# Optimization experiments

Measured on AMD Instinct MI355X. Metric: run time of the kernel, lower is better.

Reference implementation:

```python
import jax, jax.numpy as jnp
import numpy as np

HEADS = 6
K = 3       # kernel_size
PAD = 1     # padding (stride = 1, so AvgPool is identity and h=H, w=W)


def setup_inputs() -> dict:
    key = jax.random.key(0)
    ks = jax.random.split(key, 6)
    B, H, W, C = 8, 56, 56, 192
    k4h = (K ** 4) * HEADS  # 486
    s = 0.02
    return {
        "x":  jax.random.normal(ks[0], (B, H, W, C), jnp.float32),
        # weights stored as (in, out), i.e. transpose of torch nn.Linear.weight
        "Wv": jax.random.normal(ks[1], (C, C), jnp.float32) * s,
        "Wa": jax.random.normal(ks[2], (C, k4h), jnp.float32) * s,
        "ba": jnp.zeros((k4h,), jnp.float32),
        "Wp": jax.random.normal(ks[3], (C, C), jnp.float32) * s,
        "bp": jnp.zeros((C,), jnp.float32),
    }


def _outlook(x, Wv, Wa, ba, Wp, bp):
    B, H, W, C = x.shape
    hd = C // HEADS
    scale = hd ** (-0.5)
    k2 = K * K
    hw = H * W

    # v projection (no bias), to NCHW
    v = jnp.einsum("bhwc,cd->bdhw", x, Wv)                       # [B,C,H,W]

    # unfold: extract k x k local windows (same ordering as nn.Unfold: C, ki, kj)
    vp = jnp.pad(v, ((0, 0), (0, 0), (PAD, PAD), (PAD, PAD)))
    patches = jnp.stack(
        [vp[:, :, i:i + H, j:j + W] for i in range(K) for j in range(K)],
        axis=2,
    )                                                            # [B,C,k2,H,W]
    v = patches.reshape(B, HEADS, hd, k2, hw).transpose(0, 1, 4, 3, 2)  # [B,h,hw,k2,hd]

    # attention weights: dense predicted per location (pool is identity, stride=1)
    a = x.reshape(B, hw, C) @ Wa + ba                            # [B,hw,heads*k2*k2]
    a = a.reshape(B, hw, HEADS, k2, k2).transpose(0, 2, 1, 3, 4)  # [B,h,hw,k2,k2]
    a = jax.nn.softmax(a * scale, axis=-1)

    out = jnp.einsum("bnpkq,bnpqd->bnpkd", a, v)                 # [B,h,hw,k2,hd]

    # fold (col2im): scatter-add overlapping windows back, stride=1
    cols = out.transpose(0, 1, 4, 3, 2).reshape(B, C, K, K, H, W)
    acc = jnp.zeros((B, C, H + 2 * PAD, W + 2 * PAD), x.dtype)
    for i in range(K):
        for j in range(K):
            acc = acc.at[:, :, i:i + H, j:j + W].add(cols[:, :, i, j])
    y = acc[:, :, PAD:PAD + H, PAD:PAD + W].transpose(0, 2, 3, 1)  # [B,H,W,C]

    return y @ Wp + bp


def reference(x, Wv, Wa, ba, Wp, bp):
    return _outlook(x, Wv, Wa, ba, Wp, bp)
```

## Files before the change

kernel.cpp:

```cpp
#include <hip/hip_runtime.h>
#include <hip/hip_bf16.h>
#include <cstdint>

#define DI __device__ __forceinline__

typedef __attribute__((ext_vector_type(8))) short short8;
typedef __attribute__((ext_vector_type(4))) float f32x4;

DI float bflo(uint32_t u) { return __builtin_bit_cast(float, (uint32_t)(u << 16)); }
DI float bfhi(uint32_t u) { return __builtin_bit_cast(float, (uint32_t)(u & 0xffff0000u)); }
DI float bf2f(uint16_t u) { return __builtin_bit_cast(float, (uint32_t)((uint32_t)u << 16)); }
DI uint32_t cvtpk(float lo, float hi) {
    uint32_t r;
    asm("v_cvt_pk_bf16_f32 %0, %1, %2" : "=v"(r) : "v"(lo), "v"(hi));
    return r;
}
DI void gload16(const void* g, void* s) {
    __builtin_amdgcn_global_load_lds(
        (const __attribute__((address_space(1))) uint32_t*)g,
        (__attribute__((address_space(3))) uint32_t*)s, 16, 0, 0);
}
DI int xcd_swizzle(int orig, int nwg) {
    const int q = nwg >> 3, r = nwg & 7;
    const int x = orig & 7, i = orig >> 3;
    return (x < r ? x * (q + 1) : r * (q + 1) + (x - r) * q) + i;
}

constexpr int BATCH = 8, HH_IMG = 56, WW_IMG = 56, C = 192;
constexpr int HEADS = 6, HD = 32, NA = 486;
constexpr int MROWS = BATCH * HH_IMG * WW_IMG;
constexpr int KK = 192;
constexpr int TILE_B  = 49152;
constexpr int PANEL_B = 49152;


__global__ __launch_bounds__(256) void prep_all(const float* __restrict__ x,
                                                const float* __restrict__ Wv,
                                                const float* __restrict__ Wa,
                                                const float* __restrict__ Wp,
                                                uint8_t* __restrict__ xbf,
                                                uint8_t* __restrict__ WT) {
    const int bid = blockIdx.x;
    if (bid < 2352) {
        const int g = bid * 256 + threadIdx.x;
        const int m = g / 24, cc = g % 24;
        const int ks = cc >> 2, lg = cc & 3;
        const float* src = x + (size_t)m * KK + cc * 8;
        const float4 v0 = *(const float4*)src;
        const float4 v1 = *(const float4*)(src + 4);
        uint4 o;
        o.x = cvtpk(v0.x, v0.y); o.y = cvtpk(v0.z, v0.w);
        o.z = cvtpk(v1.x, v1.y); o.w = cvtpk(v1.z, v1.w);
        const size_t off = (size_t)(m >> 7) * PANEL_B +
                           ((((m >> 4) & 7) * 6 + ks) * 64 + (lg << 4) + (m & 15)) * 16;
        *(uint4*)(xbf + off) = o;
    } else {
        const int tid = (bid - 2352) * 256 + threadIdx.x;
        const int s = tid % 24, rem = tid / 24;
        const int p = rem & 127, tile = rem >> 7;
        const int lc = (p >> 5) * 32 + 2 * (p & 15) + ((p >> 4) & 1);
        const int u  = (tile < 6 ? tile : tile - 6) * 128 + lc;
        const float* src = nullptr; int nc = 0, col = 0;
        if (tile < 6) {
            if (u < 192)      { src = Wv; nc = 192; col = u; }
            else if (u < 678) { src = Wa; nc = NA;  col = u - 192; }
        } else {
            if (u < 192)      { src = Wp; nc = 192; col = u; }
        }
        const int k0 = s * 8;
        uint32_t d[4];
#pragma unroll
        for (int e = 0; e < 4; ++e) {
            const float f0 = src ? src[(size_t)(k0 + 2 * e) * nc + col]     : 0.f;
            const float f1 = src ? src[(size_t)(k0 + 2 * e + 1) * nc + col] : 0.f;
            d[e] = cvtpk(f0, f1);
        }
        const int sb = (s * 16) ^ ((p & 7) << 4);
        *(uint4*)(WT + (size_t)tile * TILE_B + p * 384 + sb) =
            make_uint4(d[0], d[1], d[2], d[3]);
    }
}

template <bool OUT_DUAL, int NT>
__global__ __launch_bounds__(256, 2) void gemm_fr(
    const uint8_t* __restrict__ Afr,
    const uint8_t* __restrict__ WT,
    uint16_t* __restrict__ vOut, uint16_t* __restrict__ alogOut,
    const float* __restrict__ bias,
    float* __restrict__ outf) {
    __shared__ __align__(16) uint8_t sm[TILE_B];
    const int t    = threadIdx.x;
    const int wgid = xcd_swizzle(blockIdx.x, gridDim.x);
    const int mg   = wgid / NT, ti = wgid - mg * NT;
    const int m0   = mg * 128;
    const int l    = t & 63, wid = t >> 6;
    const int wr   = wid >> 1, wc = wid & 1;
    const int lr   = l & 15, lg = l >> 4;

    const uint8_t* wt = WT + (size_t)ti * TILE_B;
#pragma unroll
    for (int i = 0; i < 12; ++i) {
        const int off = wid * 12288 + i * 1024;
        gload16(wt + off + l * 16, sm + off);
    }

    const uint8_t* ap = Afr + (size_t)mg * PANEL_B;
    short8 aR[6][4];
#pragma unroll
    for (int ks = 0; ks < 6; ++ks)
#pragma unroll
        for (int mr = 0; mr < 4; ++mr) {
            const int r = wr * 4 + mr;
            aR[ks][mr] = *(const short8*)(ap + (size_t)(((r * 6 + ks) * 64) + l) * 16);
        }
    __syncthreads();

    f32x4 acc[4][4];
#pragma unroll
    for (int mr = 0; mr < 4; ++mr)
#pragma unroll
        for (int nr = 0; nr < 4; ++nr) acc[mr][nr] = f32x4{0.f, 0.f, 0.f, 0.f};
#pragma unroll
    for (int ks = 0; ks < 6; ++ks) {
        const int cb = ks * 64 + lg * 16;
        short8 b[4];
#pragma unroll
        for (int nr = 0; nr < 4; ++nr) {
            const int rn = wc * 64 + nr * 16 + lr;
            b[nr] = *(const short8*)(sm + rn * 384 + (cb ^ ((rn & 7) << 4)));
        }
#pragma unroll
        for (int mr = 0; mr < 4; ++mr)
#pragma unroll
            for (int nr = 0; nr < 4; ++nr)
                acc[mr][nr] = __builtin_amdgcn_mfma_f32_16x16x32_bf16(
                    aR[ks][mr], b[nr], acc[mr][nr], 0, 0, 0);
    }

    const int gcol0 = ti * 128 + wc * 64;
#pragma unroll
    for (int pr = 0; pr < 2; ++pr) {
        if (OUT_DUAL) {
            const bool isv = gcol0 < 192;
            uint16_t* dst = isv ? vOut : alogOut;
            const int nc  = isv ? 192 : NA;
            const int c   = (isv ? gcol0 : gcol0 - 192) + pr * 32 + 2 * lr;
            if (c < nc) {
                const float be = isv ? 0.f : bias[c];
                const float bo = isv ? 0.f : bias[c + 1];
#pragma unroll
                for (int mr = 0; mr < 4; ++mr) {
                    const size_t rb = (size_t)(m0 + wr * 64 + mr * 16 + lg * 4);
#pragma unroll
                    for (int j = 0; j < 4; ++j)
                        *(uint32_t*)(dst + (rb + j) * nc + c) =
                            cvtpk(acc[mr][2 * pr][j] + be, acc[mr][2 * pr + 1][j] + bo);
                }
            }
        } else {
            const int c = gcol0 + pr * 32 + 2 * lr;
            if (c < 192) {
                const float be = bias[c], bo = bias[c + 1];
#pragma unroll
                for (int mr = 0; mr < 4; ++mr) {
                    const size_t rb = (size_t)(m0 + wr * 64 + mr * 16 + lg * 4);
#pragma unroll
                    for (int j = 0; j < 4; ++j)
                        *(float2*)(outf + (rb + j) * 192 + c) =
                            make_float2(acc[mr][2 * pr][j] + be,
                                        acc[mr][2 * pr + 1][j] + bo);
                }
            }
        }
    }
}

constexpr int TH = 4, TW = 8;
constexpr int HALO_W = TW + 4;
constexpr int VSTR = C + 8;

__global__ __launch_bounds__(192) void attn_fold25(const uint16_t* __restrict__ v,
                                                   const uint16_t* __restrict__ alog,
                                                   uint8_t* __restrict__ ypre) {
    __shared__ uint16_t vl[96][VSTR];
    const int b   = blockIdx.z;
    const int ty0 = blockIdx.y * TH, tx0 = blockIdx.x * TW;
    const int t   = threadIdx.x;

#pragma unroll
    for (int it = 0; it < 12; ++it) {
        const int f  = t + it * 192;
        const int px = f / 24, c8 = (f % 24) * 8;
        const int hy = px / HALO_W, hx = px % HALO_W;
        const int y = ty0 + hy - 2, x = tx0 + hx - 2;
        uint4 val = make_uint4(0u, 0u, 0u, 0u);
        if ((unsigned)y < HH_IMG && (unsigned)x < WW_IMG)
            val = *(const uint4*)&v[(((size_t)b * HH_IMG + y) * WW_IMG + x) * C + c8];
        *(uint4*)&vl[px][c8] = val;
    }

    const int n   = t % HEADS, pxl = t / HEADS;
    const int py  = pxl / TW, px_ = pxl % TW;
    const int Py  = ty0 + py, Px = tx0 + px_;
    const float scl2 = 0.17677669529663687f * 1.4426950408889634f;

    float cw[5][5] = {};
#pragma unroll
    for (int i = 0; i < 3; ++i)
#pragma unroll
        for (int j = 0; j < 3; ++j) {
            const int sy = Py - i + 1, sx = Px - j + 1;
            if ((unsigned)sy < HH_IMG && (unsigned)sx < WW_IMG) {
                const uint16_t* ap = alog + (((size_t)b * HH_IMG + sy) * WW_IMG + sx) * NA
                                   + n * 81 + (i * 3 + j) * 9;
                float w[9], s = 0.f;
#pragma unroll
                for (int q = 0; q < 9; ++q) {
                    w[q] = __builtin_amdgcn_exp2f(bf2f(ap[q]) * scl2);
                    s += w[q];
                }
                const float inv = __builtin_amdgcn_rcpf(s);
#pragma unroll
                for (int qi = 0; qi < 3; ++qi)
#pragma unroll
                    for (int qj = 0; qj < 3; ++qj)
                        cw[qi - i + 2][qj - j + 2] += w[qi * 3 + qj] * inv;
            }
        }
    __syncthreads();

    float acc[HD] = {};
#pragma unroll
    for (int dy = 0; dy < 5; ++dy)
#pragma unroll
        for (int dx = 0; dx < 5; ++dx) {
            const float wq = cw[dy][dx];
            const uint16_t* vp = &vl[(py + dy) * HALO_W + (px_ + dx)][n * HD];
#pragma unroll
            for (int v8 = 0; v8 < 4; ++v8) {
                const uint4 raw = *(const uint4*)&vp[v8 * 8];
                const uint32_t r0 = raw.x, r1 = raw.y, r2 = raw.z, r3 = raw.w;
                acc[v8*8+0] = fmaf(wq, bflo(r0), acc[v8*8+0]);
                acc[v8*8+1] = fmaf(wq, bfhi(r0), acc[v8*8+1]);
                acc[v8*8+2] = fmaf(wq, bflo(r1), acc[v8*8+2]);
                acc[v8*8+3] = fmaf(wq, bfhi(r1), acc[v8*8+3]);
                acc[v8*8+4] = fmaf(wq, bflo(r2), acc[v8*8+4]);
                acc[v8*8+5] = fmaf(wq, bfhi(r2), acc[v8*8+5]);
                acc[v8*8+6] = fmaf(wq, bflo(r3), acc[v8*8+6]);
                acc[v8*8+7] = fmaf(wq, bfhi(r3), acc[v8*8+7]);
            }
        }

    const int Pidx = (b * HH_IMG + Py) * WW_IMG + Px;
    uint8_t* pb = ypre + (size_t)(Pidx >> 7) * PANEL_B +
                  ((((Pidx >> 4) & 7) * 6 + n) * 64 + (Pidx & 15)) * 16;
#pragma unroll
    for (int g2 = 0; g2 < 4; ++g2) {
        uint4 o;
        o.x = cvtpk(acc[g2 * 8 + 0], acc[g2 * 8 + 1]);
        o.y = cvtpk(acc[g2 * 8 + 2], acc[g2 * 8 + 3]);
        o.z = cvtpk(acc[g2 * 8 + 4], acc[g2 * 8 + 5]);
        o.w = cvtpk(acc[g2 * 8 + 6], acc[g2 * 8 + 7]);
        *(uint4*)(pb + g2 * 256) = o;
    }
}

extern "C" void kernel_launch(void* const* d_in, const int* in_sizes, int n_in,
                              void* d_out, int out_size, void* d_ws, size_t ws_size,
                              hipStream_t stream) {
    const float* x  = (const float*)d_in[0];
    const float* Wv = (const float*)d_in[1];
    const float* Wa = (const float*)d_in[2];
    const float* ba = (const float*)d_in[3];
    const float* Wp = (const float*)d_in[4];
    const float* bp = (const float*)d_in[5];
    float* out = (float*)d_out;

    uint16_t* v    = (uint16_t*)d_ws;
    uint16_t* alog = v + (size_t)MROWS * C;
    uint8_t*  ypre = (uint8_t*)(alog + (size_t)MROWS * NA);
    uint8_t*  WT   = ypre + (size_t)(MROWS / 128) * PANEL_B;
    uint8_t*  xbf  = WT + 8 * (size_t)TILE_B;

    prep_all<<<2448, 256, 0, stream>>>(x, Wv, Wa, Wp, xbf, WT);
    gemm_fr<true, 6><<<(MROWS / 128) * 6, 256, 0, stream>>>(
        xbf, WT, v, alog, ba, nullptr);
    attn_fold25<<<dim3(WW_IMG / TW, HH_IMG / TH, BATCH), dim3(192), 0, stream>>>(
        v, alog, ypre);
    gemm_fr<false, 2><<<(MROWS / 128) * 2, 256, 0, stream>>>(
        ypre, WT + 6 * (size_t)TILE_B, nullptr, nullptr, bp, out);
}
```

Baseline: 61.64 us.

## Fuse output projection GEMM into attention-fold kernel and pad attention logits

The final Wp projection is now done inside the attention/fold kernel. Each block stages its 32 bf16 output rows in LDS and runs MFMA against a pre-fragmented Wp read from global memory, which removes the ypre round trip and one kernel launch. The attention logits are padded from 81 to 88 per head (528 columns) so each window's 9 logits load as two 16-byte vector loads instead of scalar bf16 loads. In exchange, the fused kernel needs more LDS and registers, which may lower occupancy, and every block re-reads Wp fragments from global memory.

```diff
diff --git a/kernel.cpp b/kernel.cpp
--- a/kernel.cpp
+++ b/kernel.cpp
@@ -9,7 +9,6 @@
 
 DI float bflo(uint32_t u) { return __builtin_bit_cast(float, (uint32_t)(u << 16)); }
 DI float bfhi(uint32_t u) { return __builtin_bit_cast(float, (uint32_t)(u & 0xffff0000u)); }
-DI float bf2f(uint16_t u) { return __builtin_bit_cast(float, (uint32_t)((uint32_t)u << 16)); }
 DI uint32_t cvtpk(float lo, float hi) {
     uint32_t r;
     asm("v_cvt_pk_bf16_f32 %0, %1, %2" : "=v"(r) : "v"(lo), "v"(hi));
@@ -28,18 +27,22 @@
 
 constexpr int BATCH = 8, HH_IMG = 56, WW_IMG = 56, C = 192;
 constexpr int HEADS = 6, HD = 32, NA = 486;
+constexpr int NAP = 528;
 constexpr int MROWS = BATCH * HH_IMG * WW_IMG;
 constexpr int KK = 192;
 constexpr int TILE_B  = 49152;
 constexpr int PANEL_B = 49152;
-
+constexpr int WTB_B   = 73728;
 
 __global__ __launch_bounds__(256) void prep_all(const float* __restrict__ x,
                                                 const float* __restrict__ Wv,
                                                 const float* __restrict__ Wa,
                                                 const float* __restrict__ Wp,
+                                                const float* __restrict__ ba,
                                                 uint8_t* __restrict__ xbf,
-                                                uint8_t* __restrict__ WT) {
+                                                uint8_t* __restrict__ WT,
+                                                uint8_t* __restrict__ WTB,
+                                                float* __restrict__ baP) {
     const int bid = blockIdx.x;
     if (bid < 2352) {
         const int g = bid * 256 + threadIdx.x;
@@ -54,18 +57,20 @@
         const size_t off = (size_t)(m >> 7) * PANEL_B +
                            ((((m >> 4) & 7) * 6 + ks) * 64 + (lg << 4) + (m & 15)) * 16;
         *(uint4*)(xbf + off) = o;
-    } else {
-        const int tid = (bid - 2352) * 256 + threadIdx.x;
+        return;
+    }
+    const int tid = (bid - 2352) * 256 + threadIdx.x;
+    if (tid < 18432) {
         const int s = tid % 24, rem = tid / 24;
         const int p = rem & 127, tile = rem >> 7;
         const int lc = (p >> 5) * 32 + 2 * (p & 15) + ((p >> 4) & 1);
-        const int u  = (tile < 6 ? tile : tile - 6) * 128 + lc;
+        const int u  = tile * 128 + lc;
         const float* src = nullptr; int nc = 0, col = 0;
-        if (tile < 6) {
-            if (u < 192)      { src = Wv; nc = 192; col = u; }
-            else if (u < 678) { src = Wa; nc = NA;  col = u - 192; }
-        } else {
-            if (u < 192)      { src = Wp; nc = 192; col = u; }
+        if (u < 192) { src = Wv; nc = 192; col = u; }
+        else if (u < 720) {
+            const int up = u - 192;
+            const int head = up / 88, r88 = up - head * 88;
+            if (r88 < 81) { src = Wa; nc = NA; col = head * 81 + r88; }
         }
         const int k0 = s * 8;
         uint32_t d[4];
@@ -78,20 +83,37 @@
         const int sb = (s * 16) ^ ((p & 7) << 4);
         *(uint4*)(WT + (size_t)tile * TILE_B + p * 384 + sb) =
             make_uint4(d[0], d[1], d[2], d[3]);
-    }
-}
-
-template <bool OUT_DUAL, int NT>
+    } else if (tid < 18432 + 4608) {
+        const int g = tid - 18432;
+        const int l = g & 63, gg = g >> 6;
+        const int ks = gg % 6, nrIdx = gg / 6;
+        const int pp = nrIdx >> 1, h = nrIdx & 1;
+        const int col = pp * 32 + 2 * (l & 15) + h;
+        const int k0  = ks * 32 + (l >> 4) * 8;
+        uint32_t d[4];
+#pragma unroll
+        for (int e = 0; e < 4; ++e) {
+            const float f0 = Wp[(size_t)(k0 + 2 * e) * 192 + col];
+            const float f1 = Wp[(size_t)(k0 + 2 * e + 1) * 192 + col];
+            d[e] = cvtpk(f0, f1);
+        }
+        *(uint4*)(WTB + (size_t)g * 16) = make_uint4(d[0], d[1], d[2], d[3]);
+    } else if (tid < 18432 + 4608 + NAP) {
+        const int pc = tid - 18432 - 4608;
+        const int head = pc / 88, r88 = pc - head * 88;
+        baP[pc] = (r88 < 81) ? ba[head * 81 + r88] : 0.f;
+    }
+}
+
 __global__ __launch_bounds__(256, 2) void gemm_fr(
     const uint8_t* __restrict__ Afr,
     const uint8_t* __restrict__ WT,
-    uint16_t* __restrict__ vOut, uint16_t* __restrict__ alogOut,
-    const float* __restrict__ bias,
-    float* __restrict__ outf) {
+    uint16_t* __restrict__ zOut, uint16_t* __restrict__ alogP,
+    const float* __restrict__ baP) {
     __shared__ __align__(16) uint8_t sm[TILE_B];
     const int t    = threadIdx.x;
     const int wgid = xcd_swizzle(blockIdx.x, gridDim.x);
-    const int mg   = wgid / NT, ti = wgid - mg * NT;
+    const int mg   = wgid / 6, ti = wgid - mg * 6;
     const int m0   = mg * 128;
     const int l    = t & 63, wid = t >> 6;
     const int wr   = wid >> 1, wc = wid & 1;
@@ -140,35 +162,27 @@
     const int gcol0 = ti * 128 + wc * 64;
 #pragma unroll
     for (int pr = 0; pr < 2; ++pr) {
-        if (OUT_DUAL) {
-            const bool isv = gcol0 < 192;
-            uint16_t* dst = isv ? vOut : alogOut;
-            const int nc  = isv ? 192 : NA;
-            const int c   = (isv ? gcol0 : gcol0 - 192) + pr * 32 + 2 * lr;
-            if (c < nc) {
-                const float be = isv ? 0.f : bias[c];
-                const float bo = isv ? 0.f : bias[c + 1];
+        const int uc = gcol0 + pr * 32 + 2 * lr;
+        if (uc < 192) {
+#pragma unroll
+            for (int mr = 0; mr < 4; ++mr) {
+                const size_t rb = (size_t)(m0 + wr * 64 + mr * 16 + lg * 4);
+#pragma unroll
+                for (int j = 0; j < 4; ++j)
+                    *(uint32_t*)(zOut + (rb + j) * 192 + uc) =
+                        cvtpk(acc[mr][2 * pr][j], acc[mr][2 * pr + 1][j]);
+            }
+        } else {
+            const int pc = uc - 192;
+            if (pc < NAP) {
+                const float be = baP[pc], bo = baP[pc + 1];
 #pragma unroll
                 for (int mr = 0; mr < 4; ++mr) {
                     const size_t rb = (size_t)(m0 + wr * 64 + mr * 16 + lg * 4);
 #pragma unroll
                     for (int j = 0; j < 4; ++j)
-                        *(uint32_t*)(dst + (rb + j) * nc + c) =
+                        *(uint32_t*)(alogP + (rb + j) * NAP + pc) =
                             cvtpk(acc[mr][2 * pr][j] + be, acc[mr][2 * pr + 1][j] + bo);
-                }
-            }
-        } else {
-            const int c = gcol0 + pr * 32 + 2 * lr;
-            if (c < 192) {
-                const float be = bias[c], bo = bias[c + 1];
-#pragma unroll
-                for (int mr = 0; mr < 4; ++mr) {
-                    const size_t rb = (size_t)(m0 + wr * 64 + mr * 16 + lg * 4);
-#pragma unroll
-                    for (int j = 0; j < 4; ++j)
-                        *(float2*)(outf + (rb + j) * 192 + c) =
-                            make_float2(acc[mr][2 * pr][j] + be,
-                                        acc[mr][2 * pr + 1][j] + bo);
                 }
             }
         }
@@ -178,11 +192,16 @@
 constexpr int TH = 4, TW = 8;
 constexpr int HALO_W = TW + 4;
 constexpr int VSTR = C + 8;
-
-__global__ __launch_bounds__(192) void attn_fold25(const uint16_t* __restrict__ v,
-                                                   const uint16_t* __restrict__ alog,
-                                                   uint8_t* __restrict__ ypre) {
-    __shared__ uint16_t vl[96][VSTR];
+constexpr int YL_OFF = 96 * VSTR * 2;
+
+__global__ __launch_bounds__(192) void attn_fused(const uint16_t* __restrict__ z,
+                                                  const uint16_t* __restrict__ alogP,
+                                                  const uint8_t* __restrict__ WTB,
+                                                  const float* __restrict__ bp,
+                                                  float* __restrict__ out) {
+    __shared__ __align__(16) uint8_t smem[YL_OFF + 32 * 384];
+    uint16_t (*vl)[VSTR] = (uint16_t(*)[VSTR])smem;
+    uint8_t* yl = smem + YL_OFF;
     const int b   = blockIdx.z;
     const int ty0 = blockIdx.y * TH, tx0 = blockIdx.x * TW;
     const int t   = threadIdx.x;
@@ -195,12 +214,12 @@
         const int y = ty0 + hy - 2, x = tx0 + hx - 2;
         uint4 val = make_uint4(0u, 0u, 0u, 0u);
         if ((unsigned)y < HH_IMG && (unsigned)x < WW_IMG)
-            val = *(const uint4*)&v[(((size_t)b * HH_IMG + y) * WW_IMG + x) * C + c8];
+            val = *(const uint4*)&z[(((size_t)b * HH_IMG + y) * WW_IMG + x) * C + c8];
         *(uint4*)&vl[px][c8] = val;
     }
 
     const int n   = t % HEADS, pxl = t / HEADS;
-    const int py  = pxl / TW, px_ = pxl % TW;
+    const int py  = pxl >> 3, px_ = pxl & 7;
     const int Py  = ty0 + py, Px = tx0 + px_;
     const float scl2 = 0.17677669529663687f * 1.4426950408889634f;
 
@@ -211,12 +230,20 @@
         for (int j = 0; j < 3; ++j) {
             const int sy = Py - i + 1, sx = Px - j + 1;
             if ((unsigned)sy < HH_IMG && (unsigned)sx < WW_IMG) {
-                const uint16_t* ap = alog + (((size_t)b * HH_IMG + sy) * WW_IMG + sx) * NA
-                                   + n * 81 + (i * 3 + j) * 9;
+                const uint8_t* rp = (const uint8_t*)alogP +
+                    (((size_t)b * HH_IMG + sy) * WW_IMG + sx) * (NAP * 2) + n * 176;
+                const int win = i * 3 + j;
+                const int off = win * 18, a0 = off & ~15, base = off - a0;
+                const uint4 u0 = *(const uint4*)(rp + a0);
+                const uint4 u1 = *(const uint4*)(rp + a0 + 16);
+                const uint32_t dd[8] = {u0.x, u0.y, u0.z, u0.w, u1.x, u1.y, u1.z, u1.w};
                 float w[9], s = 0.f;
 #pragma unroll
                 for (int q = 0; q < 9; ++q) {
-                    w[q] = __builtin_amdgcn_exp2f(bf2f(ap[q]) * scl2);
+                    const int bb = base + 2 * q;
+                    const uint32_t dw = dd[bb >> 2];
+                    const float f0 = (bb & 2) ? bfhi(dw) : bflo(dw);
+                    w[q] = __builtin_amdgcn_exp2f(f0 * scl2);
                     s += w[q];
                 }
                 const float inv = __builtin_amdgcn_rcpf(s);
@@ -251,17 +278,67 @@
             }
         }
 
-    const int Pidx = (b * HH_IMG + Py) * WW_IMG + Px;
-    uint8_t* pb = ypre + (size_t)(Pidx >> 7) * PANEL_B +
-                  ((((Pidx >> 4) & 7) * 6 + n) * 64 + (Pidx & 15)) * 16;
-#pragma unroll
-    for (int g2 = 0; g2 < 4; ++g2) {
-        uint4 o;
-        o.x = cvtpk(acc[g2 * 8 + 0], acc[g2 * 8 + 1]);
-        o.y = cvtpk(acc[g2 * 8 + 2], acc[g2 * 8 + 3]);
-        o.z = cvtpk(acc[g2 * 8 + 4], acc[g2 * 8 + 5]);
-        o.w = cvtpk(acc[g2 * 8 + 6], acc[g2 * 8 + 7]);
-        *(uint4*)(pb + g2 * 256) = o;
+    {
+        uint8_t* pb = yl + pxl * 384;
+        const int key = (pxl & 7) << 4;
+#pragma unroll
+        for (int g2 = 0; g2 < 4; ++g2) {
+            uint4 o;
+            o.x = cvtpk(acc[g2 * 8 + 0], acc[g2 * 8 + 1]);
+            o.y = cvtpk(acc[g2 * 8 + 2], acc[g2 * 8 + 3]);
+            o.z = cvtpk(acc[g2 * 8 + 4], acc[g2 * 8 + 5]);
+            o.w = cvtpk(acc[g2 * 8 + 6], acc[g2 * 8 + 7]);
+            *(uint4*)(pb + ((n * 64 + g2 * 16) ^ key)) = o;
+        }
+    }
+    __syncthreads();
+
+    const int l = t & 63, wid = t >> 6;
+    const int lr = l & 15, lg = l >> 4;
+    short8 aF[2][6];
+#pragma unroll
+    for (int r = 0; r < 2; ++r)
+#pragma unroll
+        for (int ks = 0; ks < 6; ++ks) {
+            const int row = r * 16 + lr;
+            aF[r][ks] = *(const short8*)(yl + row * 384 +
+                          ((ks * 64 + lg * 16) ^ ((row & 7) << 4)));
+        }
+    f32x4 gacc[2][4];
+#pragma unroll
+    for (int r = 0; r < 2; ++r)
+#pragma unroll
+        for (int f = 0; f < 4; ++f) gacc[r][f] = f32x4{0.f, 0.f, 0.f, 0.f};
+#pragma unroll
+    for (int ks = 0; ks < 6; ++ks) {
+        short8 bF[4];
+#pragma unroll
+        for (int f = 0; f < 4; ++f) {
+            const int nrIdx = wid * 4 + f;
+            bF[f] = *(const short8*)(WTB + (size_t)(((nrIdx * 6 + ks) * 64) + l) * 16);
+        }
+#pragma unroll
+        for (int r = 0; r < 2; ++r)
+#pragma unroll
+            for (int f = 0; f < 4; ++f)
+                gacc[r][f] = __builtin_amdgcn_mfma_f32_16x16x32_bf16(
+                    aF[r][ks], bF[f], gacc[r][f], 0, 0, 0);
+    }
+
+#pragma unroll
+    for (int pi = 0; pi < 2; ++pi) {
+        const int col = wid * 64 + pi * 32 + 2 * lr;
+        const float be = bp[col], bo = bp[col + 1];
+#pragma unroll
+        for (int r = 0; r < 2; ++r)
+#pragma unroll
+            for (int j = 0; j < 4; ++j) {
+                const int prow = r * 16 + lg * 4 + j;
+                const int gy = ty0 + (prow >> 3), gx = tx0 + (prow & 7);
+                float* op = out + (((size_t)b * HH_IMG + gy) * WW_IMG + gx) * C + col;
+                *(float2*)op = make_float2(gacc[r][2 * pi][j] + be,
+                                           gacc[r][2 * pi + 1][j] + bo);
+            }
     }
 }
 
@@ -276,17 +353,15 @@
     const float* bp = (const float*)d_in[5];
     float* out = (float*)d_out;
 
-    uint16_t* v    = (uint16_t*)d_ws;
-    uint16_t* alog = v + (size_t)MROWS * C;
-    uint8_t*  ypre = (uint8_t*)(alog + (size_t)MROWS * NA);
-    uint8_t*  WT   = ypre + (size_t)(MROWS / 128) * PANEL_B;
-    uint8_t*  xbf  = WT + 8 * (size_t)TILE_B;
-
-    prep_all<<<2448, 256, 0, stream>>>(x, Wv, Wa, Wp, xbf, WT);
-    gemm_fr<true, 6><<<(MROWS / 128) * 6, 256, 0, stream>>>(
-        xbf, WT, v, alog, ba, nullptr);
-    attn_fold25<<<dim3(WW_IMG / TW, HH_IMG / TH, BATCH), dim3(192), 0, stream>>>(
-        v, alog, ypre);
-    gemm_fr<false, 2><<<(MROWS / 128) * 2, 256, 0, stream>>>(
-        ypre, WT + 6 * (size_t)TILE_B, nullptr, nullptr, bp, out);
-}
+    uint16_t* z     = (uint16_t*)d_ws;
+    uint16_t* alogP = z + (size_t)MROWS * C;
+    uint8_t*  xbf   = (uint8_t*)(alogP + (size_t)MROWS * NAP);
+    uint8_t*  WT    = xbf + (size_t)(MROWS / 128) * PANEL_B;
+    uint8_t*  WTB   = WT + 6 * (size_t)TILE_B;
+    float*    baP   = (float*)(WTB + WTB_B);
+
+    prep_all<<<2352 + 93, 256, 0, stream>>>(x, Wv, Wa, Wp, ba, xbf, WT, WTB, baP);
+    gemm_fr<<<(MROWS / 128) * 6, 256, 0, stream>>>(xbf, WT, z, alogP, baP);
+    attn_fused<<<dim3(WW_IMG / TW, HH_IMG / TH, BATCH), dim3(192), 0, stream>>>(
+        z, alogP, WTB, bp, out);
+}
```

After: 60.87 us. About the same (-1.2%).
